# Kernel tuning notes

Hardware: AMD Instinct MI355X
Metric: run time of the kernel (lower is better)

Reference implementation:

```python
import jax, jax.numpy as jnp
import numpy as np

N, P, T, D = 25000, 100000, 4, 128
DIN = 4 * D + 4  # 516
LEAKY = 0.001


def setup_inputs() -> dict:
    key = jax.random.key(0)
    ks = jax.random.split(key, 12)
    inp = {
        "coords": jax.random.normal(ks[0], (N, T, 3), jnp.float32),
        "propers": jax.random.randint(ks[1], (P, 4), 0, N, jnp.int64),
        "encoded": jax.random.normal(ks[2], (N, D), jnp.float32),
        "t": jax.random.uniform(ks[3], (T,), jnp.float32),
        "answer": jax.random.normal(ks[4], (N, T, 3), jnp.float32),
        # AggregateMLP(516 -> 128 -> 128 -> 128 -> 2), LeakyReLU(0.001) between
        "W0": jax.random.normal(ks[5], (DIN, D), jnp.float32) / np.sqrt(DIN),
        "b0": jnp.zeros((D,), jnp.float32),
        "W1": jax.random.normal(ks[6], (D, D), jnp.float32) / np.sqrt(D),
        "b1": jnp.zeros((D,), jnp.float32),
        "W2": jax.random.normal(ks[7], (D, D), jnp.float32) / np.sqrt(D),
        "b2": jnp.zeros((D,), jnp.float32),
        "W3": jax.random.normal(ks[8], (D, 2), jnp.float32) / np.sqrt(D),
        "b3": jnp.zeros((2,), jnp.float32),
    }
    return inp


def _forward(coords, propers, encoded, t, answer, W0, b0, W1, b1, W2, b2, W3, b3):
    p0, p1, p2, p3 = propers[:, 0], propers[:, 1], propers[:, 2], propers[:, 3]
    c0, c1, c2, c3 = coords[p0], coords[p1], coords[p2], coords[p3]  # [P,T,3]
    u1 = c1 - c0
    u2 = c2 - c1
    u3 = c3 - c2
    u1xu2 = jnp.cross(u1, u2, axis=-1)
    u2xu3 = jnp.cross(u2, u3, axis=-1)
    u2_norm = jnp.linalg.norm(u2, axis=-1, keepdims=True)
    u1yu2 = u1 * u2_norm
    theta = jnp.arctan2((u1yu2 * u2xu3).sum(-1), (u1xu2 * u2xu3).sum(-1))  # [P,T]
    dr = c0 - c3  # [P,T,3]
    dl = jnp.sqrt(jnp.clip(jnp.square(dr).sum(-1), 1e-12))  # [P,T]
    dh = dr / dl[..., None]

    Pn, Tn = propers.shape[0], t.shape[0]
    bcast = lambda e: jnp.broadcast_to(e[:, None, :], (Pn, Tn, e.shape[-1]))
    feats = jnp.concatenate(
        [
            bcast(encoded[p0]),
            bcast(encoded[p1]),
            bcast(encoded[p2]),
            bcast(encoded[p3]),
            jnp.broadcast_to(t.reshape(1, Tn, 1), (Pn, Tn, 1)),
            jnp.sin(theta)[..., None],
            jnp.cos(theta)[..., None],
            dl[..., None],
        ],
        axis=2,
    )  # [P,T,516]

    h = jax.nn.leaky_relu(feats @ W0 + b0, LEAKY)
    h = jax.nn.leaky_relu(h @ W1 + b1, LEAKY)
    h = jax.nn.leaky_relu(h @ W2 + b2, LEAKY)
    delta = h @ W3 + b3  # [P,T,2]

    out = answer.at[p0].add(-0.5 * delta[:, :, 0:1] * dh)
    out = out.at[p3].add(0.5 * delta[:, :, 1:2] * dh)
    return out


def reference(coords, propers, encoded, t, answer, W0, b0, W1, b1, W2, b2, W3, b3):
    return _forward(coords, propers, encoded, t, answer, W0, b0, W1, b1, W2, b2, W3, b3)
```

## Files before the change

kernel.cpp:

```cpp
#include <hip/hip_runtime.h>
#include <hip/hip_bf16.h>

#define NN 25000
#define PP 100000
#define TT 4
#define DD 128
#define LEAKY 0.001f

#define PB 32
#define ROWS 128

typedef __bf16 bf16;
typedef __bf16 bf16x8 __attribute__((ext_vector_type(8)));
typedef float  f32x4  __attribute__((ext_vector_type(4)));

#define OFF_ENCB  0u
#define OFF_W0SW  6400000u
#define OFF_W1SW  6531072u
#define OFF_W2SW  6563840u
#define OFF_W3SW  6596608u
#define OFF_E     6600704u
#define WS_END    32200704u

#define PR_ENCB4 800000
#define PR_W0SW  65536
#define PR_W1SW  16384
#define PR_W2SW  16384
#define PR_W3SW  2048
#define PR_COPY4 75000
#define PR_TOTAL (PR_ENCB4 + PR_W0SW + PR_W1SW + PR_W2SW + PR_W3SW + PR_COPY4)

__global__ __launch_bounds__(256) void prep_kernel(
    const float* __restrict__ encoded, const float* __restrict__ W0,
    const float* __restrict__ W1, const float* __restrict__ W2,
    const float* __restrict__ W3, const float* __restrict__ answer,
    bf16* __restrict__ encB, bf16* __restrict__ W0sw, bf16* __restrict__ W1sw,
    bf16* __restrict__ W2sw, bf16* __restrict__ W3sw, float* __restrict__ out)
{
    int idx = blockIdx.x * 256 + threadIdx.x;
    if (idx < PR_ENCB4) {
        float4 v = ((const float4*)encoded)[idx];
        bf16 pk[4] = {(bf16)v.x, (bf16)v.y, (bf16)v.z, (bf16)v.w};
        *(uint2*)(encB + idx * 4) = *(const uint2*)pk;
        return;
    }
    idx -= PR_ENCB4;
    if (idx < PR_W0SW) {
        int j = idx & 7, lane = (idx >> 3) & 63, c = idx >> 9;
        int fr = lane & 15, quad = lane >> 4;
        int kc = c & 15, iwv = c >> 4;
        int k = kc * 32 + quad * 8 + j;
        W0sw[idx] = (bf16)W0[k * 128 + iwv * 16 + fr];
        return;
    }
    idx -= PR_W0SW;
    if (idx < PR_W1SW) {
        int j = idx & 7, lane = (idx >> 3) & 63, c = idx >> 9;
        int fr = lane & 15, quad = lane >> 4;
        int kc = c & 3, nt = c >> 2;
        int k = kc * 32 + quad * 8 + j;
        W1sw[idx] = (bf16)W1[k * 128 + nt * 16 + fr];
        return;
    }
    idx -= PR_W1SW;
    if (idx < PR_W2SW) {
        int j = idx & 7, lane = (idx >> 3) & 63, c = idx >> 9;
        int fr = lane & 15, quad = lane >> 4;
        int kc = c & 3, nt = c >> 2;
        int k = kc * 32 + quad * 8 + j;
        W2sw[idx] = (bf16)W2[k * 128 + nt * 16 + fr];
        return;
    }
    idx -= PR_W2SW;
    if (idx < PR_W3SW) {
        int j = idx & 7, lane = (idx >> 3) & 63, kc = idx >> 9;
        int fr = lane & 15, quad = lane >> 4;
        int k = kc * 32 + quad * 8 + j;
        W3sw[idx] = (fr < 2) ? (bf16)W3[k * 2 + fr] : (bf16)0.0f;
        return;
    }
    idx -= PR_W3SW;
    if (idx < PR_COPY4) { ((float4*)out)[idx] = ((const float4*)answer)[idx]; }
}

__global__ __launch_bounds__(512, 4) void prep_e_kernel(
    const bf16* __restrict__ encB, const bf16* __restrict__ W0sw,
    bf16* __restrict__ E)
{
    __shared__ bf16 sA[16][136];
    const int tid = threadIdx.x;
    const int row0 = blockIdx.x * 16;
    if (tid < 256) {
        int row = tid >> 4, seg = tid & 15;
        int rr = row0 + row; if (rr > NN - 1) rr = NN - 1;
        *(bf16x8*)(&sA[row][seg * 8]) =
            *(const bf16x8*)(encB + (size_t)rr * 128 + seg * 8);
    }
    __syncthreads();
    const int wv = tid >> 6, lane = tid & 63;
    const int fr = lane & 15, quad = lane >> 4;
    const bf16* aBase = &sA[fr][quad * 8];
    #pragma unroll
    for (int i = 0; i < 4; ++i) {
        f32x4 dacc = {0.f, 0.f, 0.f, 0.f};
        #pragma unroll
        for (int kcc = 0; kcc < 4; ++kcc) {
            bf16x8 aF = *(const bf16x8*)(aBase + kcc * 32);
            bf16x8 bF = *(const bf16x8*)(W0sw + ((size_t)wv * 16 + i * 4 + kcc) * 512 + lane * 8);
            dacc = __builtin_amdgcn_mfma_f32_16x16x32_bf16(aF, bF, dacc, 0, 0, 0);
        }
        #pragma unroll
        for (int reg = 0; reg < 4; ++reg) {
            int row = row0 + quad * 4 + reg;
            if (row < NN)
                E[((size_t)i * NN + row) * 128 + wv * 16 + fr] = (bf16)dacc[reg];
        }
    }
}

__global__ __launch_bounds__(512, 4) void main_kernel(
    const float* __restrict__ coords, const int* __restrict__ propers,
    const float* __restrict__ tvec, const float* __restrict__ W0,
    const float* __restrict__ b0, const float* __restrict__ b1,
    const float* __restrict__ b2, const float* __restrict__ b3,
    const bf16* __restrict__ E, const bf16* __restrict__ W1sw,
    const bf16* __restrict__ W2sw, const bf16* __restrict__ W3sw,
    float* __restrict__ out)
{
    __shared__ bf16 sBuf0[ROWS * 136];
    __shared__ bf16 sBuf1[ROWS * 136];
    #define SH0(r, j) sBuf0[(r) * 136 + (j)]
    #define SH1(r, j) sBuf1[(r) * 136 + (j)]
    __shared__ int   sNodes[PB][4];
    __shared__ float sSn[ROWS], sCs[ROWS], sDl[ROWS], sDh[ROWS][3];
    __shared__ float sDelta[ROWS][2];

    const int tid  = threadIdx.x;
    const int pBase = blockIdx.x * PB;
    const float tv0 = tvec[0], tv1 = tvec[1], tv2 = tvec[2], tv3 = tvec[3];

    const int p  = tid >> 4, s8 = tid & 15;
    bf16x8 e0, e1, e2, e3;
    float w512v[8], w513v[8], w514v[8], w515v[8], b0v[8];
    {
        const int* prow = propers + (pBase + p) * 4;
        int n0 = prow[0], n1 = prow[1], n2 = prow[2], n3 = prow[3];
        e0 = *(const bf16x8*)(E + ((size_t)0 * NN + n0) * 128 + s8 * 8);
        e1 = *(const bf16x8*)(E + ((size_t)1 * NN + n1) * 128 + s8 * 8);
        e2 = *(const bf16x8*)(E + ((size_t)2 * NN + n2) * 128 + s8 * 8);
        e3 = *(const bf16x8*)(E + ((size_t)3 * NN + n3) * 128 + s8 * 8);
        *(float4*)(w512v)     = *(const float4*)(W0 + 512 * 128 + s8 * 8);
        *(float4*)(w512v + 4) = *(const float4*)(W0 + 512 * 128 + s8 * 8 + 4);
        *(float4*)(w513v)     = *(const float4*)(W0 + 513 * 128 + s8 * 8);
        *(float4*)(w513v + 4) = *(const float4*)(W0 + 513 * 128 + s8 * 8 + 4);
        *(float4*)(w514v)     = *(const float4*)(W0 + 514 * 128 + s8 * 8);
        *(float4*)(w514v + 4) = *(const float4*)(W0 + 514 * 128 + s8 * 8 + 4);
        *(float4*)(w515v)     = *(const float4*)(W0 + 515 * 128 + s8 * 8);
        *(float4*)(w515v + 4) = *(const float4*)(W0 + 515 * 128 + s8 * 8 + 4);
        *(float4*)(b0v)       = *(const float4*)(b0 + s8 * 8);
        *(float4*)(b0v + 4)   = *(const float4*)(b0 + s8 * 8 + 4);
    }
    if (tid < PB * 4) sNodes[tid >> 2][tid & 3] = propers[(pBase + (tid >> 2)) * 4 + (tid & 3)];
    if (tid < ROWS) {
        int r = tid, pp = r >> 2, t = r & 3;
        const int* prow = propers + (pBase + pp) * 4;
        int n0 = prow[0], n1 = prow[1], n2 = prow[2], n3 = prow[3];
        const float* c0 = coords + n0 * 12 + t * 3;
        const float* c1 = coords + n1 * 12 + t * 3;
        const float* c2 = coords + n2 * 12 + t * 3;
        const float* c3 = coords + n3 * 12 + t * 3;
        float u1x = c1[0]-c0[0], u1y = c1[1]-c0[1], u1z = c1[2]-c0[2];
        float u2x = c2[0]-c1[0], u2y = c2[1]-c1[1], u2z = c2[2]-c1[2];
        float u3x = c3[0]-c2[0], u3y = c3[1]-c2[1], u3z = c3[2]-c2[2];
        float ax = u1y*u2z - u1z*u2y, ay = u1z*u2x - u1x*u2z, az = u1x*u2y - u1y*u2x;
        float bx = u2y*u3z - u2z*u3y, by = u2z*u3x - u2x*u3z, bz = u2x*u3y - u2y*u3x;
        float u2n = sqrtf(u2x*u2x + u2y*u2y + u2z*u2z);
        float num = u2n * (u1x*bx + u1y*by + u1z*bz);
        float den = ax*bx + ay*by + az*bz;
        float hyp = sqrtf(num*num + den*den);
        float sn, cs;
        if (hyp > 1e-30f) { float ih = 1.0f / hyp; sn = num * ih; cs = den * ih; }
        else { sn = 0.0f; cs = 1.0f; }
        float drx = c0[0]-c3[0], dry = c0[1]-c3[1], drz = c0[2]-c3[2];
        float dl = sqrtf(fmaxf(drx*drx + dry*dry + drz*drz, 1e-12f));
        float il = 1.0f / dl;
        sSn[r] = sn; sCs[r] = cs; sDl[r] = dl;
        sDh[r][0] = drx * il; sDh[r][1] = dry * il; sDh[r][2] = drz * il;
    }
    __syncthreads();

    {
        float g[8];
        #pragma unroll
        for (int j = 0; j < 8; ++j)
            g[j] = (float)e0[j] + (float)e1[j] + (float)e2[j] + (float)e3[j] + b0v[j];
        #pragma unroll
        for (int t = 0; t < 4; ++t) {
            int r = p * 4 + t;
            float tvv = (t == 0) ? tv0 : (t == 1) ? tv1 : (t == 2) ? tv2 : tv3;
            float sn = sSn[r], cs = sCs[r], dl = sDl[r];
            bf16 hv[8];
            #pragma unroll
            for (int j = 0; j < 8; ++j) {
                float v = g[j] + tvv * w512v[j] + sn * w513v[j] + cs * w514v[j] + dl * w515v[j];
                v = fmaxf(v, LEAKY * v);
                hv[j] = (bf16)v;
            }
            *(bf16x8*)(&SH0(r, s8 * 8)) = *(const bf16x8*)hv;
        }
    }
    __syncthreads();

    const int wv = tid >> 6, lane = tid & 63;
    const int fr = lane & 15, quad = lane >> 4;
    const int m2 = (wv & 3) * 2;
    const int nh = wv >> 2;

    #pragma unroll
    for (int s = 0; s < 2; ++s) {
        f32x4 hacc[4];
        #pragma unroll
        for (int nt = 0; nt < 4; ++nt) hacc[nt] = (f32x4){0.f,0.f,0.f,0.f};
        const bf16* aRow = &SH0((m2 + s) * 16 + fr, quad * 8);
        const bf16* w1b = W1sw + lane * 8;
        #pragma unroll
        for (int kc = 0; kc < 4; ++kc) {
            bf16x8 aF = *(const bf16x8*)(aRow + kc * 32);
            #pragma unroll
            for (int nt = 0; nt < 4; ++nt) {
                bf16x8 bF = *(const bf16x8*)(w1b + ((nh * 4 + nt) * 4 + kc) * 512);
                hacc[nt] = __builtin_amdgcn_mfma_f32_16x16x32_bf16(aF, bF, hacc[nt], 0, 0, 0);
            }
        }
        #pragma unroll
        for (int nt = 0; nt < 4; ++nt) {
            int j = (nh * 4 + nt) * 16 + fr;
            float bb = b1[j];
            #pragma unroll
            for (int reg = 0; reg < 4; ++reg) {
                int r = (m2 + s) * 16 + quad * 4 + reg;
                float v = hacc[nt][reg] + bb;
                v = fmaxf(v, LEAKY * v);
                SH1(r, j) = (bf16)v;
            }
        }
    }
    __syncthreads();

    #pragma unroll
    for (int s = 0; s < 2; ++s) {
        f32x4 hacc[4];
        #pragma unroll
        for (int nt = 0; nt < 4; ++nt) hacc[nt] = (f32x4){0.f,0.f,0.f,0.f};
        const bf16* aRow = &SH1((m2 + s) * 16 + fr, quad * 8);
        const bf16* w2b = W2sw + lane * 8;
        #pragma unroll
        for (int kc = 0; kc < 4; ++kc) {
            bf16x8 aF = *(const bf16x8*)(aRow + kc * 32);
            #pragma unroll
            for (int nt = 0; nt < 4; ++nt) {
                bf16x8 bF = *(const bf16x8*)(w2b + ((nh * 4 + nt) * 4 + kc) * 512);
                hacc[nt] = __builtin_amdgcn_mfma_f32_16x16x32_bf16(aF, bF, hacc[nt], 0, 0, 0);
            }
        }
        #pragma unroll
        for (int nt = 0; nt < 4; ++nt) {
            int j = (nh * 4 + nt) * 16 + fr;
            float bb = b2[j];
            #pragma unroll
            for (int reg = 0; reg < 4; ++reg) {
                int r = (m2 + s) * 16 + quad * 4 + reg;
                float v = hacc[nt][reg] + bb;
                v = fmaxf(v, LEAKY * v);
                SH0(r, j) = (bf16)v;
            }
        }
    }
    __syncthreads();

    {
        f32x4 dacc = {0.f,0.f,0.f,0.f};
        const bf16* aRow = &SH0(wv * 16 + fr, quad * 8);
        const bf16* w3b = W3sw + lane * 8;
        #pragma unroll
        for (int kc = 0; kc < 4; ++kc) {
            bf16x8 aF = *(const bf16x8*)(aRow + kc * 32);
            bf16x8 bF = *(const bf16x8*)(w3b + kc * 512);
            dacc = __builtin_amdgcn_mfma_f32_16x16x32_bf16(aF, bF, dacc, 0, 0, 0);
        }
        if (fr < 2) {
            float bb = b3[fr];
            #pragma unroll
            for (int reg = 0; reg < 4; ++reg)
                sDelta[wv * 16 + quad * 4 + reg][fr] = dacc[reg] + bb;
        }
    }
    __syncthreads();

    for (int idx = tid; idx < ROWS * 6; idx += 512) {
        int r = idx / 6, c = idx % 6;
        int pp = r >> 2, t = r & 3;
        int side = c / 3, ax = c % 3;
        int node = sNodes[pp][side ? 3 : 0];
        float dval = side ? 0.5f * sDelta[r][1] : -0.5f * sDelta[r][0];
        atomicAdd(out + node * 12 + t * 3 + ax, dval * sDh[r][ax]);
    }
    #undef SH0
    #undef SH1
}

extern "C" void kernel_launch(void* const* d_in, const int* in_sizes, int n_in,
                              void* d_out, int out_size, void* d_ws, size_t ws_size,
                              hipStream_t stream) {
    const float* coords  = (const float*)d_in[0];
    const int*   propers = (const int*)d_in[1];
    const float* encoded = (const float*)d_in[2];
    const float* tvec    = (const float*)d_in[3];
    const float* answer  = (const float*)d_in[4];
    const float* W0 = (const float*)d_in[5];
    const float* b0 = (const float*)d_in[6];
    const float* W1 = (const float*)d_in[7];
    const float* b1 = (const float*)d_in[8];
    const float* W2 = (const float*)d_in[9];
    const float* b2 = (const float*)d_in[10];
    const float* W3 = (const float*)d_in[11];
    const float* b3 = (const float*)d_in[12];
    float* out = (float*)d_out;
    char* ws = (char*)d_ws;
    bf16* encB = (bf16*)(ws + OFF_ENCB);
    bf16* W0sw = (bf16*)(ws + OFF_W0SW);
    bf16* W1sw = (bf16*)(ws + OFF_W1SW);
    bf16* W2sw = (bf16*)(ws + OFF_W2SW);
    bf16* W3sw = (bf16*)(ws + OFF_W3SW);
    bf16* E    = (bf16*)(ws + OFF_E);

    int prep_blocks = (PR_TOTAL + 255) / 256;
    prep_kernel<<<prep_blocks, 256, 0, stream>>>(encoded, W0, W1, W2, W3, answer,
                                                 encB, W0sw, W1sw, W2sw, W3sw, out);
    prep_e_kernel<<<(NN + 15) / 16, 512, 0, stream>>>(encB, W0sw, E);
    main_kernel<<<PP / PB, 512, 0, stream>>>(coords, propers, tvec, W0, b0, b1, b2, b3,
                                             E, W1sw, W2sw, W3sw, out);
}
```

Measured before the change: 204.9 us.

## Retile E precompute to 128-row blocks and precompute t/extra-feature weights in bf16

Result: slower. 215.6 us (+5.2%).

```diff
diff --git a/kernel.cpp b/kernel.cpp
--- a/kernel.cpp
+++ b/kernel.cpp
@@ -13,29 +13,36 @@
 typedef __bf16 bf16;
 typedef __bf16 bf16x8 __attribute__((ext_vector_type(8)));
 typedef float  f32x4  __attribute__((ext_vector_type(4)));
+typedef float  f32x2  __attribute__((ext_vector_type(2)));
 
 #define OFF_ENCB  0u
 #define OFF_W0SW  6400000u
 #define OFF_W1SW  6531072u
 #define OFF_W2SW  6563840u
 #define OFF_W3SW  6596608u
-#define OFF_E     6600704u
-#define WS_END    32200704u
+#define OFF_WTB   6600704u
+#define OFF_W5B   6601728u
+#define OFF_E     6602496u
+#define WS_END    32202496u
 
 #define PR_ENCB4 800000
 #define PR_W0SW  65536
 #define PR_W1SW  16384
 #define PR_W2SW  16384
 #define PR_W3SW  2048
+#define PR_WTB   512
+#define PR_W5B   384
 #define PR_COPY4 75000
-#define PR_TOTAL (PR_ENCB4 + PR_W0SW + PR_W1SW + PR_W2SW + PR_W3SW + PR_COPY4)
+#define PR_TOTAL (PR_ENCB4 + PR_W0SW + PR_W1SW + PR_W2SW + PR_W3SW + PR_WTB + PR_W5B + PR_COPY4)
 
 __global__ __launch_bounds__(256) void prep_kernel(
     const float* __restrict__ encoded, const float* __restrict__ W0,
     const float* __restrict__ W1, const float* __restrict__ W2,
     const float* __restrict__ W3, const float* __restrict__ answer,
+    const float* __restrict__ tvec,
     bf16* __restrict__ encB, bf16* __restrict__ W0sw, bf16* __restrict__ W1sw,
-    bf16* __restrict__ W2sw, bf16* __restrict__ W3sw, float* __restrict__ out)
+    bf16* __restrict__ W2sw, bf16* __restrict__ W3sw, bf16* __restrict__ WtB,
+    bf16* __restrict__ W5B, float* __restrict__ out)
 {
     int idx = blockIdx.x * 256 + threadIdx.x;
     if (idx < PR_ENCB4) {
@@ -80,51 +87,67 @@
         return;
     }
     idx -= PR_W3SW;
+    if (idx < PR_WTB) {
+        int t = idx >> 7, j = idx & 127;
+        WtB[idx] = (bf16)(tvec[t] * W0[512 * 128 + j]);
+        return;
+    }
+    idx -= PR_WTB;
+    if (idx < PR_W5B) {
+        W5B[idx] = (bf16)W0[(513 + (idx >> 7)) * 128 + (idx & 127)];
+        return;
+    }
+    idx -= PR_W5B;
     if (idx < PR_COPY4) { ((float4*)out)[idx] = ((const float4*)answer)[idx]; }
 }
 
-__global__ __launch_bounds__(512, 4) void prep_e_kernel(
+__global__ __launch_bounds__(512) void prep_e_kernel(
     const bf16* __restrict__ encB, const bf16* __restrict__ W0sw,
     bf16* __restrict__ E)
 {
-    __shared__ bf16 sA[16][136];
+    __shared__ bf16 sA[128][136];
     const int tid = threadIdx.x;
-    const int row0 = blockIdx.x * 16;
-    if (tid < 256) {
-        int row = tid >> 4, seg = tid & 15;
-        int rr = row0 + row; if (rr > NN - 1) rr = NN - 1;
+    const int row0 = blockIdx.x * 128;
+    for (int c = tid; c < 2048; c += 512) {
+        int row = c >> 4, seg = c & 15;
+        int rr = row0 + row; if (rr >= NN) rr = NN - 1;
         *(bf16x8*)(&sA[row][seg * 8]) =
             *(const bf16x8*)(encB + (size_t)rr * 128 + seg * 8);
     }
     __syncthreads();
     const int wv = tid >> 6, lane = tid & 63;
     const int fr = lane & 15, quad = lane >> 4;
-    const bf16* aBase = &sA[fr][quad * 8];
+    const bf16* aBase = &sA[wv * 16 + fr][quad * 8];
+    bf16x8 aFv[4];
+    #pragma unroll
+    for (int kcc = 0; kcc < 4; ++kcc) aFv[kcc] = *(const bf16x8*)(aBase + kcc * 32);
     #pragma unroll
     for (int i = 0; i < 4; ++i) {
-        f32x4 dacc = {0.f, 0.f, 0.f, 0.f};
-        #pragma unroll
-        for (int kcc = 0; kcc < 4; ++kcc) {
-            bf16x8 aF = *(const bf16x8*)(aBase + kcc * 32);
-            bf16x8 bF = *(const bf16x8*)(W0sw + ((size_t)wv * 16 + i * 4 + kcc) * 512 + lane * 8);
-            dacc = __builtin_amdgcn_mfma_f32_16x16x32_bf16(aF, bF, dacc, 0, 0, 0);
-        }
-        #pragma unroll
-        for (int reg = 0; reg < 4; ++reg) {
-            int row = row0 + quad * 4 + reg;
-            if (row < NN)
-                E[((size_t)i * NN + row) * 128 + wv * 16 + fr] = (bf16)dacc[reg];
+        #pragma unroll
+        for (int nt = 0; nt < 8; ++nt) {
+            f32x4 acc = {0.f, 0.f, 0.f, 0.f};
+            #pragma unroll
+            for (int kcc = 0; kcc < 4; ++kcc) {
+                bf16x8 bF = *(const bf16x8*)(W0sw + ((size_t)nt * 16 + i * 4 + kcc) * 512 + lane * 8);
+                acc = __builtin_amdgcn_mfma_f32_16x16x32_bf16(aFv[kcc], bF, acc, 0, 0, 0);
+            }
+            #pragma unroll
+            for (int reg = 0; reg < 4; ++reg) {
+                int row = row0 + wv * 16 + quad * 4 + reg;
+                if (row < NN)
+                    E[((size_t)i * NN + row) * 128 + nt * 16 + fr] = (bf16)acc[reg];
+            }
         }
     }
 }
 
 __global__ __launch_bounds__(512, 4) void main_kernel(
     const float* __restrict__ coords, const int* __restrict__ propers,
-    const float* __restrict__ tvec, const float* __restrict__ W0,
     const float* __restrict__ b0, const float* __restrict__ b1,
     const float* __restrict__ b2, const float* __restrict__ b3,
     const bf16* __restrict__ E, const bf16* __restrict__ W1sw,
     const bf16* __restrict__ W2sw, const bf16* __restrict__ W3sw,
+    const bf16* __restrict__ WtB, const bf16* __restrict__ W5B,
     float* __restrict__ out)
 {
     __shared__ bf16 sBuf0[ROWS * 136];
@@ -137,38 +160,25 @@
 
     const int tid  = threadIdx.x;
     const int pBase = blockIdx.x * PB;
-    const float tv0 = tvec[0], tv1 = tvec[1], tv2 = tvec[2], tv3 = tvec[3];
 
     const int p  = tid >> 4, s8 = tid & 15;
     bf16x8 e0, e1, e2, e3;
-    float w512v[8], w513v[8], w514v[8], w515v[8], b0v[8];
     {
-        const int* prow = propers + (pBase + p) * 4;
-        int n0 = prow[0], n1 = prow[1], n2 = prow[2], n3 = prow[3];
-        e0 = *(const bf16x8*)(E + ((size_t)0 * NN + n0) * 128 + s8 * 8);
-        e1 = *(const bf16x8*)(E + ((size_t)1 * NN + n1) * 128 + s8 * 8);
-        e2 = *(const bf16x8*)(E + ((size_t)2 * NN + n2) * 128 + s8 * 8);
-        e3 = *(const bf16x8*)(E + ((size_t)3 * NN + n3) * 128 + s8 * 8);
-        *(float4*)(w512v)     = *(const float4*)(W0 + 512 * 128 + s8 * 8);
-        *(float4*)(w512v + 4) = *(const float4*)(W0 + 512 * 128 + s8 * 8 + 4);
-        *(float4*)(w513v)     = *(const float4*)(W0 + 513 * 128 + s8 * 8);
-        *(float4*)(w513v + 4) = *(const float4*)(W0 + 513 * 128 + s8 * 8 + 4);
-        *(float4*)(w514v)     = *(const float4*)(W0 + 514 * 128 + s8 * 8);
-        *(float4*)(w514v + 4) = *(const float4*)(W0 + 514 * 128 + s8 * 8 + 4);
-        *(float4*)(w515v)     = *(const float4*)(W0 + 515 * 128 + s8 * 8);
-        *(float4*)(w515v + 4) = *(const float4*)(W0 + 515 * 128 + s8 * 8 + 4);
-        *(float4*)(b0v)       = *(const float4*)(b0 + s8 * 8);
-        *(float4*)(b0v + 4)   = *(const float4*)(b0 + s8 * 8 + 4);
-    }
-    if (tid < PB * 4) sNodes[tid >> 2][tid & 3] = propers[(pBase + (tid >> 2)) * 4 + (tid & 3)];
+        int4 pv = *(const int4*)(propers + (pBase + p) * 4);
+        if (s8 == 0) { sNodes[p][0] = pv.x; sNodes[p][1] = pv.y;
+                       sNodes[p][2] = pv.z; sNodes[p][3] = pv.w; }
+        e0 = *(const bf16x8*)(E + ((size_t)0 * NN + pv.x) * 128 + s8 * 8);
+        e1 = *(const bf16x8*)(E + ((size_t)1 * NN + pv.y) * 128 + s8 * 8);
+        e2 = *(const bf16x8*)(E + ((size_t)2 * NN + pv.z) * 128 + s8 * 8);
+        e3 = *(const bf16x8*)(E + ((size_t)3 * NN + pv.w) * 128 + s8 * 8);
+    }
     if (tid < ROWS) {
         int r = tid, pp = r >> 2, t = r & 3;
-        const int* prow = propers + (pBase + pp) * 4;
-        int n0 = prow[0], n1 = prow[1], n2 = prow[2], n3 = prow[3];
-        const float* c0 = coords + n0 * 12 + t * 3;
-        const float* c1 = coords + n1 * 12 + t * 3;
-        const float* c2 = coords + n2 * 12 + t * 3;
-        const float* c3 = coords + n3 * 12 + t * 3;
+        int4 pv = *(const int4*)(propers + (pBase + pp) * 4);
+        const float* c0 = coords + pv.x * 12 + t * 3;
+        const float* c1 = coords + pv.y * 12 + t * 3;
+        const float* c2 = coords + pv.z * 12 + t * 3;
+        const float* c3 = coords + pv.w * 12 + t * 3;
         float u1x = c1[0]-c0[0], u1y = c1[1]-c0[1], u1z = c1[2]-c0[2];
         float u2x = c2[0]-c1[0], u2y = c2[1]-c1[1], u2z = c2[2]-c1[2];
         float u3x = c3[0]-c2[0], u3y = c3[1]-c2[1], u3z = c3[2]-c2[2];
@@ -190,21 +200,38 @@
     __syncthreads();
 
     {
-        float g[8];
-        #pragma unroll
-        for (int j = 0; j < 8; ++j)
-            g[j] = (float)e0[j] + (float)e1[j] + (float)e2[j] + (float)e3[j] + b0v[j];
+        f32x2 g2[4];
+        #pragma unroll
+        for (int j2 = 0; j2 < 4; ++j2) {
+            g2[j2].x = (float)e0[2*j2]   + (float)e1[2*j2]   + (float)e2[2*j2]   + (float)e3[2*j2];
+            g2[j2].y = (float)e0[2*j2+1] + (float)e1[2*j2+1] + (float)e2[2*j2+1] + (float)e3[2*j2+1];
+        }
+        bf16x8 w3v = *(const bf16x8*)(W5B + 0 * 128 + s8 * 8);
+        bf16x8 w4v = *(const bf16x8*)(W5B + 1 * 128 + s8 * 8);
+        bf16x8 w5v = *(const bf16x8*)(W5B + 2 * 128 + s8 * 8);
+        float b0a = b0[s8 * 8];
+        float b0v[8];
+        *(float4*)(b0v)     = *(const float4*)(b0 + s8 * 8);
+        *(float4*)(b0v + 4) = *(const float4*)(b0 + s8 * 8 + 4);
+        (void)b0a;
         #pragma unroll
         for (int t = 0; t < 4; ++t) {
             int r = p * 4 + t;
-            float tvv = (t == 0) ? tv0 : (t == 1) ? tv1 : (t == 2) ? tv2 : tv3;
+            bf16x8 wtv = *(const bf16x8*)(WtB + t * 128 + s8 * 8);
             float sn = sSn[r], cs = sCs[r], dl = sDl[r];
+            f32x2 snv = {sn, sn}, csv = {cs, cs}, dlv = {dl, dl};
             bf16 hv[8];
             #pragma unroll
-            for (int j = 0; j < 8; ++j) {
-                float v = g[j] + tvv * w512v[j] + sn * w513v[j] + cs * w514v[j] + dl * w515v[j];
-                v = fmaxf(v, LEAKY * v);
-                hv[j] = (bf16)v;
+            for (int j2 = 0; j2 < 4; ++j2) {
+                f32x2 v = g2[j2];
+                v += (f32x2){(float)wtv[2*j2] + b0v[2*j2], (float)wtv[2*j2+1] + b0v[2*j2+1]};
+                v += snv * (f32x2){(float)w3v[2*j2], (float)w3v[2*j2+1]};
+                v += csv * (f32x2){(float)w4v[2*j2], (float)w4v[2*j2+1]};
+                v += dlv * (f32x2){(float)w5v[2*j2], (float)w5v[2*j2+1]};
+                v.x = fmaxf(v.x, LEAKY * v.x);
+                v.y = fmaxf(v.y, LEAKY * v.y);
+                hv[2*j2]   = (bf16)v.x;
+                hv[2*j2+1] = (bf16)v.y;
             }
             *(bf16x8*)(&SH0(r, s8 * 8)) = *(const bf16x8*)hv;
         }
@@ -332,12 +359,14 @@
     bf16* W1sw = (bf16*)(ws + OFF_W1SW);
     bf16* W2sw = (bf16*)(ws + OFF_W2SW);
     bf16* W3sw = (bf16*)(ws + OFF_W3SW);
+    bf16* WtB  = (bf16*)(ws + OFF_WTB);
+    bf16* W5B  = (bf16*)(ws + OFF_W5B);
     bf16* E    = (bf16*)(ws + OFF_E);
 
     int prep_blocks = (PR_TOTAL + 255) / 256;
-    prep_kernel<<<prep_blocks, 256, 0, stream>>>(encoded, W0, W1, W2, W3, answer,
-                                                 encB, W0sw, W1sw, W2sw, W3sw, out);
-    prep_e_kernel<<<(NN + 15) / 16, 512, 0, stream>>>(encB, W0sw, E);
-    main_kernel<<<PP / PB, 512, 0, stream>>>(coords, propers, tvec, W0, b0, b1, b2, b3,
-                                             E, W1sw, W2sw, W3sw, out);
+    prep_kernel<<<prep_blocks, 256, 0, stream>>>(encoded, W0, W1, W2, W3, answer, tvec,
+                                                 encB, W0sw, W1sw, W2sw, W3sw, WtB, W5B, out);
+    prep_e_kernel<<<(NN + 127) / 128, 512, 0, stream>>>(encB, W0sw, E);
+    main_kernel<<<PP / PB, 512, 0, stream>>>(coords, propers, b0, b1, b2, b3,
+                                             E, W1sw, W2sw, W3sw, WtB, W5B, out);
 }
```
